# Kernel optimization log

Hardware: AMD Instinct MI355X
Metric: run time of the kernel (lower is better)

## Reference

```python
import jax, jax.numpy as jnp
import numpy as np

GRID = (8, 8)
EPS = 1e-5  # nn.BatchNorm2d default eps


def _per_tile(t, g, b, w, cb):
    # t: (B, C, th, tw); training-mode BatchNorm over (B, th, tw) per channel
    mean = t.mean(axis=(0, 2, 3))
    var = t.var(axis=(0, 2, 3))  # biased variance, matches torch BN normalization
    xn = (t - mean[:, None, None]) * jax.lax.rsqrt(var[:, None, None] + EPS)
    h = jax.nn.relu(xn * g[:, None, None] + b[:, None, None])
    y = jax.lax.conv_general_dilated(
        h, w, window_strides=(1, 1), padding='SAME',
        dimension_numbers=('NCHW', 'OIHW', 'NCHW'))
    return y + cb[:, None, None] + t  # conv bias + residual


def setup_inputs() -> dict:
    key = jax.random.key(0)
    k1, k2 = jax.random.split(key)
    B, C, H, W = 32, 32, 160, 160
    n_tiles = GRID[0] * GRID[1]
    x = jax.random.normal(k1, (B, C, H, W), dtype=jnp.float32)
    gamma = jnp.ones((n_tiles, C), dtype=jnp.float32)
    beta = jnp.zeros((n_tiles, C), dtype=jnp.float32)
    # kaiming-ish init for 3x3 conv
    conv_w = jax.random.normal(k2, (n_tiles, C, C, 3, 3), dtype=jnp.float32) * (2.0 / (C * 9)) ** 0.5
    conv_b = jnp.zeros((n_tiles, C), dtype=jnp.float32)
    return {"x": x, "gamma": gamma, "beta": beta, "conv_w": conv_w, "conv_b": conv_b}


def reference(x, gamma, beta, conv_w, conv_b):
    B, C, H, W = x.shape
    gi, gj = GRID
    th, tw = H // gi, W // gj
    # split into (gi*gj, B, C, th, tw) tiles
    tiles = x.reshape(B, C, gi, th, gj, tw).transpose(2, 4, 0, 1, 3, 5)
    tiles = tiles.reshape(gi * gj, B, C, th, tw)
    out = jax.vmap(_per_tile)(tiles, gamma, beta, conv_w, conv_b)
    # reassemble
    out = out.reshape(gi, gj, B, C, th, tw).transpose(2, 3, 0, 4, 1, 5)
    return out.reshape(B, C, H, W)
```

## Files before the change

kernel.cpp:

```cpp
#include <hip/hip_runtime.h>

#define NT 64
#define B_ 32
#define C_ 32
#define H_ 160
#define W_ 160
#define TH 20
#define TW 20
#define NPIX (TH*TW)
#define NRED (B_*NPIX)
#define EPS 1e-5f

typedef __bf16 bf16x8 __attribute__((ext_vector_type(8)));
typedef float  f32x4  __attribute__((ext_vector_type(4)));

__global__ __launch_bounds__(320) void statsA_kernel(const float* __restrict__ x,
                                                     float* __restrict__ ppS,
                                                     float* __restrict__ ppS2) {
    int blk = blockIdx.x;
    int b = blk >> 5;
    int c = blk & 31;
    const float* plane = x + ((long)(b*C_ + c)) * H_ * W_;

    int tid = threadIdx.x;
    int col4 = tid % 40;
    int tc   = col4 / 5;
    int rbase = tid / 40;

    __shared__ float sh[320], sh2[320], shr[64], shr2[64];

    for (int tr = 0; tr < 8; ++tr) {
        float s = 0.f, s2 = 0.f;
        #pragma unroll
        for (int k = 0; k < 3; ++k) {
            int i = tid + 320*k;
            if (i < 800) {
                int row = tr*20 + rbase + 8*k;
                const float* p = plane + row*W_ + col4*4;
                float4 v = *(const float4*)p;
                s  += v.x + v.y + v.z + v.w;
                s2 += v.x*v.x + v.y*v.y + v.z*v.z + v.w*v.w;
            }
        }
        sh[tid] = s; sh2[tid] = s2;
        __syncthreads();
        if (tid < 64) {
            int tcc = tid >> 3, sl = tid & 7;
            float ps = 0.f, ps2 = 0.f;
            #pragma unroll
            for (int r = 0; r < 5; ++r) {
                int t = sl*40 + tcc*5 + r;
                ps += sh[t]; ps2 += sh2[t];
            }
            shr[tid] = ps; shr2[tid] = ps2;
        }
        __syncthreads();
        if (tid < 8) {
            float ps = 0.f, ps2 = 0.f;
            #pragma unroll
            for (int sl = 0; sl < 8; ++sl) { ps += shr[tid*8 + sl]; ps2 += shr2[tid*8 + sl]; }
            int tl = tr*8 + tid;
            atomicAdd(&ppS [tl*C_ + c], ps);
            atomicAdd(&ppS2[tl*C_ + c], ps2);
        }
        __syncthreads();
    }
}

__global__ __launch_bounds__(512, 4) void fused_kernel(
        const float* __restrict__ x,
        const float* __restrict__ gamma,
        const float* __restrict__ beta,
        const float* __restrict__ conv_w,
        const float* __restrict__ conv_b,
        const float* __restrict__ ppS,
        const float* __restrict__ ppS2,
        float* __restrict__ out) {
    int blk = blockIdx.x;
    int tl = blk >> 5;
    int b  = blk & 31;
    int ti = (tl >> 3) * TH;
    int tj = (tl & 7)  * TW;
    int tid = threadIdx.x;

    __shared__ __align__(16) unsigned char smem[75776];
    __bf16* hlds  = (__bf16*)smem;
    __bf16* wlds  = (__bf16*)(smem + 30976);
    __bf16* obuf  = (__bf16*)(smem + 49408);
    float*  scale = (float*)(smem + 75520);
    float*  shiftv= (float*)(smem + 75648);

    {
        unsigned int* hz = (unsigned int*)smem;
        for (int i = tid; i < 7744; i += 512) hz[i] = 0u;
    }
    if (tid < C_) {
        int c = tid;
        float s  = ppS [tl*C_ + c];
        float s2 = ppS2[tl*C_ + c];
        float m  = s / (float)NRED;
        float var = s2 / (float)NRED - m*m;
        float rs = rsqrtf(var + EPS);
        float g  = gamma[tl*C_ + c];
        scale[c]  = g * rs;
        shiftv[c] = beta[tl*C_ + c] - m * rs * g;
    }
    {
        const float* wsrc = conv_w + (long)tl * C_ * C_ * 9;
        for (int f = tid; f < C_*C_*9; f += 512) {
            int co  = f / 288;
            int rem = f - co*288;
            int cin = rem / 9;
            int tap = rem - cin*9;
            wlds[(tap*C_ + co)*C_ + cin] = (__bf16)wsrc[f];
        }
    }
    __syncthreads();

    for (int idx = tid; idx < C_*TH*5; idx += 512) {
        int c   = idx / 100;
        int rem = idx - c*100;
        int y   = rem / 5;
        int x4  = rem - y*5;
        const float* p = x + ((long)(b*C_ + c)*H_ + ti + y)*W_ + tj + x4*4;
        float4 v = *(const float4*)p;
        float sc = scale[c], sf = shiftv[c];
        int base = ((y+1)*22 + (x4*4 + 1)) * C_ + c;
        hlds[base        ] = (__bf16)fmaxf(v.x*sc + sf, 0.f);
        hlds[base + C_   ] = (__bf16)fmaxf(v.y*sc + sf, 0.f);
        hlds[base + 2*C_ ] = (__bf16)fmaxf(v.z*sc + sf, 0.f);
        hlds[base + 3*C_ ] = (__bf16)fmaxf(v.w*sc + sf, 0.f);
    }
    __syncthreads();

    int wv   = tid >> 6;
    int lane = tid & 63;
    int mm   = lane & 15;
    int j0   = (lane >> 4) * 8;

    bf16x8 bfr[9][2];
    #pragma unroll
    for (int tap = 0; tap < 9; ++tap) {
        #pragma unroll
        for (int h = 0; h < 2; ++h)
            bfr[tap][h] = *(const bf16x8*)&wlds[(tap*C_ + (h*16 + mm))*C_ + j0];
    }
    float b0 = conv_b[tl*C_ + mm];
    float b1 = conv_b[tl*C_ + 16 + mm];

    for (int chunk = wv; chunk < 25; chunk += 8) {
        int p  = chunk*16 + mm;
        int py = p / 20;
        int px = p - py*20;
        f32x4 a0, a1;
        #pragma unroll
        for (int r = 0; r < 4; ++r) { a0[r] = b0; a1[r] = b1; }
        #pragma unroll
        for (int ky = 0; ky < 3; ++ky) {
            #pragma unroll
            for (int kx = 0; kx < 3; ++kx) {
                bf16x8 af = *(const bf16x8*)&hlds[((py+ky)*22 + (px+kx))*C_ + j0];
                a0 = __builtin_amdgcn_mfma_f32_16x16x32_bf16(af, bfr[ky*3+kx][0], a0, 0, 0, 0);
                a1 = __builtin_amdgcn_mfma_f32_16x16x32_bf16(af, bfr[ky*3+kx][1], a1, 0, 0, 0);
            }
        }
        #pragma unroll
        for (int r = 0; r < 4; ++r) {
            int pix = chunk*16 + (lane >> 4)*4 + r;
            obuf[mm*408 + pix]        = (__bf16)a0[r];
            obuf[(16 + mm)*408 + pix] = (__bf16)a1[r];
        }
    }
    __syncthreads();

    for (int idx = tid; idx < C_*NPIX; idx += 512) {
        int co = idx / NPIX;
        int p  = idx - co*NPIX;
        int y  = p / 20;
        int xx = p - y*20;
        long o = ((long)(b*C_ + co)*H_ + ti + y)*W_ + tj + xx;
        out[o] = (float)obuf[co*408 + p] + x[o];
    }
}

extern "C" void kernel_launch(void* const* d_in, const int* in_sizes, int n_in,
                              void* d_out, int out_size, void* d_ws, size_t ws_size,
                              hipStream_t stream) {
    const float* x      = (const float*)d_in[0];
    const float* gamma  = (const float*)d_in[1];
    const float* beta   = (const float*)d_in[2];
    const float* conv_w = (const float*)d_in[3];
    const float* conv_b = (const float*)d_in[4];
    float* out = (float*)d_out;

    float* ppS  = (float*)d_ws;
    float* ppS2 = ppS + NT*C_;

    hipMemsetAsync(d_ws, 0, 2 * NT * C_ * sizeof(float), stream);
    statsA_kernel<<<B_ * C_, 320, 0, stream>>>(x, ppS, ppS2);
    fused_kernel<<<NT * B_, 512, 0, stream>>>(x, gamma, beta, conv_w, conv_b,
                                              ppS, ppS2, out);
}
```

Baseline: 301.3 us.

## Pad LDS strides, alias weight/output buffers, vectorize epilogue and stats reduction

```diff
diff --git a/kernel.cpp b/kernel.cpp
--- a/kernel.cpp
+++ b/kernel.cpp
@@ -11,7 +11,11 @@
 #define NRED (B_*NPIX)
 #define EPS 1e-5f
 
+#define HP 40
+#define OP 404
+
 typedef __bf16 bf16x8 __attribute__((ext_vector_type(8)));
+typedef __bf16 bf16x4 __attribute__((ext_vector_type(4)));
 typedef float  f32x4  __attribute__((ext_vector_type(4)));
 
 __global__ __launch_bounds__(320) void statsA_kernel(const float* __restrict__ x,
@@ -22,48 +26,44 @@
     int c = blk & 31;
     const float* plane = x + ((long)(b*C_ + c)) * H_ * W_;
 
-    int tid = threadIdx.x;
-    int col4 = tid % 40;
-    int tc   = col4 / 5;
+    int tid   = threadIdx.x;
+    int col4  = tid % 40;
     int rbase = tid / 40;
 
-    __shared__ float sh[320], sh2[320], shr[64], shr2[64];
-
+    __shared__ float sh [8 * 321];
+    __shared__ float sh2[8 * 321];
+
+    #pragma unroll
     for (int tr = 0; tr < 8; ++tr) {
         float s = 0.f, s2 = 0.f;
         #pragma unroll
         for (int k = 0; k < 3; ++k) {
-            int i = tid + 320*k;
-            if (i < 800) {
-                int row = tr*20 + rbase + 8*k;
-                const float* p = plane + row*W_ + col4*4;
-                float4 v = *(const float4*)p;
+            int r20 = rbase + 8*k;
+            if (r20 < 20) {
+                int row = tr*20 + r20;
+                float4 v = *(const float4*)(plane + row*W_ + col4*4);
                 s  += v.x + v.y + v.z + v.w;
                 s2 += v.x*v.x + v.y*v.y + v.z*v.z + v.w*v.w;
             }
         }
-        sh[tid] = s; sh2[tid] = s2;
-        __syncthreads();
-        if (tid < 64) {
-            int tcc = tid >> 3, sl = tid & 7;
-            float ps = 0.f, ps2 = 0.f;
+        sh [tr*321 + tid] = s;
+        sh2[tr*321 + tid] = s2;
+    }
+    __syncthreads();
+
+    if (tid < 64) {
+        int tr = tid >> 3, tc = tid & 7;
+        float ps = 0.f, ps2 = 0.f;
+        #pragma unroll
+        for (int rb = 0; rb < 8; ++rb)
             #pragma unroll
-            for (int r = 0; r < 5; ++r) {
-                int t = sl*40 + tcc*5 + r;
+            for (int c5 = 0; c5 < 5; ++c5) {
+                int t = tr*321 + rb*40 + tc*5 + c5;
                 ps += sh[t]; ps2 += sh2[t];
             }
-            shr[tid] = ps; shr2[tid] = ps2;
-        }
-        __syncthreads();
-        if (tid < 8) {
-            float ps = 0.f, ps2 = 0.f;
-            #pragma unroll
-            for (int sl = 0; sl < 8; ++sl) { ps += shr[tid*8 + sl]; ps2 += shr2[tid*8 + sl]; }
-            int tl = tr*8 + tid;
-            atomicAdd(&ppS [tl*C_ + c], ps);
-            atomicAdd(&ppS2[tl*C_ + c], ps2);
-        }
-        __syncthreads();
+        int tl = tr*8 + tc;
+        atomicAdd(&ppS [tl*C_ + c], ps);
+        atomicAdd(&ppS2[tl*C_ + c], ps2);
     }
 }
 
@@ -83,25 +83,25 @@
     int tj = (tl & 7)  * TW;
     int tid = threadIdx.x;
 
-    __shared__ __align__(16) unsigned char smem[75776];
-    __bf16* hlds  = (__bf16*)smem;
-    __bf16* wlds  = (__bf16*)(smem + 30976);
-    __bf16* obuf  = (__bf16*)(smem + 49408);
-    float*  scale = (float*)(smem + 75520);
-    float*  shiftv= (float*)(smem + 75648);
+    __shared__ __align__(16) unsigned char smem[64832];
+    __bf16* hlds   = (__bf16*)smem;
+    __bf16* wlds   = (__bf16*)(smem + 38720);
+    __bf16* obuf   = (__bf16*)(smem + 38720);
+    float*  scale  = (float*)(smem + 64576);
+    float*  shiftv = (float*)(smem + 64704);
 
     {
-        unsigned int* hz = (unsigned int*)smem;
-        for (int i = tid; i < 7744; i += 512) hz[i] = 0u;
+        uint4* hz = (uint4*)smem;
+        for (int i = tid; i < 2420; i += 512) hz[i] = uint4{0,0,0,0};
     }
     if (tid < C_) {
         int c = tid;
-        float s  = ppS [tl*C_ + c];
-        float s2 = ppS2[tl*C_ + c];
-        float m  = s / (float)NRED;
+        float s   = ppS [tl*C_ + c];
+        float s2  = ppS2[tl*C_ + c];
+        float m   = s / (float)NRED;
         float var = s2 / (float)NRED - m*m;
-        float rs = rsqrtf(var + EPS);
-        float g  = gamma[tl*C_ + c];
+        float rs  = rsqrtf(var + EPS);
+        float g   = gamma[tl*C_ + c];
         scale[c]  = g * rs;
         shiftv[c] = beta[tl*C_ + c] - m * rs * g;
     }
@@ -112,7 +112,7 @@
             int rem = f - co*288;
             int cin = rem / 9;
             int tap = rem - cin*9;
-            wlds[(tap*C_ + co)*C_ + cin] = (__bf16)wsrc[f];
+            wlds[(tap*C_ + co)*HP + cin] = (__bf16)wsrc[f];
         }
     }
     __syncthreads();
@@ -125,28 +125,30 @@
         const float* p = x + ((long)(b*C_ + c)*H_ + ti + y)*W_ + tj + x4*4;
         float4 v = *(const float4*)p;
         float sc = scale[c], sf = shiftv[c];
-        int base = ((y+1)*22 + (x4*4 + 1)) * C_ + c;
-        hlds[base        ] = (__bf16)fmaxf(v.x*sc + sf, 0.f);
-        hlds[base + C_   ] = (__bf16)fmaxf(v.y*sc + sf, 0.f);
-        hlds[base + 2*C_ ] = (__bf16)fmaxf(v.z*sc + sf, 0.f);
-        hlds[base + 3*C_ ] = (__bf16)fmaxf(v.w*sc + sf, 0.f);
-    }
-    __syncthreads();
-
+        int base = ((y+1)*22 + (x4*4 + 1)) * HP + c;
+        hlds[base         ] = (__bf16)fmaxf(v.x*sc + sf, 0.f);
+        hlds[base +   HP  ] = (__bf16)fmaxf(v.y*sc + sf, 0.f);
+        hlds[base + 2*HP  ] = (__bf16)fmaxf(v.z*sc + sf, 0.f);
+        hlds[base + 3*HP  ] = (__bf16)fmaxf(v.w*sc + sf, 0.f);
+    }
+    __syncthreads();
+
+    int lane = tid & 63;
     int wv   = tid >> 6;
-    int lane = tid & 63;
     int mm   = lane & 15;
-    int j0   = (lane >> 4) * 8;
+    int jg   = lane >> 4;
+    int j0   = jg * 8;
 
     bf16x8 bfr[9][2];
     #pragma unroll
     for (int tap = 0; tap < 9; ++tap) {
         #pragma unroll
         for (int h = 0; h < 2; ++h)
-            bfr[tap][h] = *(const bf16x8*)&wlds[(tap*C_ + (h*16 + mm))*C_ + j0];
+            bfr[tap][h] = *(const bf16x8*)&wlds[(tap*C_ + (h*16 + mm))*HP + j0];
     }
     float b0 = conv_b[tl*C_ + mm];
     float b1 = conv_b[tl*C_ + 16 + mm];
+    __syncthreads();
 
     for (int chunk = wv; chunk < 25; chunk += 8) {
         int p  = chunk*16 + mm;
@@ -159,27 +161,34 @@
         for (int ky = 0; ky < 3; ++ky) {
             #pragma unroll
             for (int kx = 0; kx < 3; ++kx) {
-                bf16x8 af = *(const bf16x8*)&hlds[((py+ky)*22 + (px+kx))*C_ + j0];
+                bf16x8 af = *(const bf16x8*)&hlds[((py+ky)*22 + (px+kx))*HP + j0];
                 a0 = __builtin_amdgcn_mfma_f32_16x16x32_bf16(af, bfr[ky*3+kx][0], a0, 0, 0, 0);
                 a1 = __builtin_amdgcn_mfma_f32_16x16x32_bf16(af, bfr[ky*3+kx][1], a1, 0, 0, 0);
             }
         }
-        #pragma unroll
-        for (int r = 0; r < 4; ++r) {
-            int pix = chunk*16 + (lane >> 4)*4 + r;
-            obuf[mm*408 + pix]        = (__bf16)a0[r];
-            obuf[(16 + mm)*408 + pix] = (__bf16)a1[r];
-        }
-    }
-    __syncthreads();
-
-    for (int idx = tid; idx < C_*NPIX; idx += 512) {
-        int co = idx / NPIX;
-        int p  = idx - co*NPIX;
-        int y  = p / 20;
-        int xx = p - y*20;
-        long o = ((long)(b*C_ + co)*H_ + ti + y)*W_ + tj + xx;
-        out[o] = (float)obuf[co*408 + p] + x[o];
+        bf16x4 o0, o1;
+        #pragma unroll
+        for (int r = 0; r < 4; ++r) { o0[r] = (__bf16)a0[r]; o1[r] = (__bf16)a1[r]; }
+        int pb = chunk*16 + jg*4;
+        *(bf16x4*)&obuf[mm*OP + pb]        = o0;
+        *(bf16x4*)&obuf[(16 + mm)*OP + pb] = o1;
+    }
+    __syncthreads();
+
+    for (int idx = tid; idx < C_*NPIX/4; idx += 512) {
+        int co = idx / 100;
+        int q  = idx - co*100;
+        int y  = q / 5;
+        int x4 = q - y*5;
+        bf16x4 v = *(const bf16x4*)&obuf[co*OP + y*20 + x4*4];
+        long o = (((long)(b*C_ + co))*H_ + ti + y)*W_ + tj + x4*4;
+        float4 xr = *(const float4*)&x[o];
+        float4 ov;
+        ov.x = (float)v[0] + xr.x;
+        ov.y = (float)v[1] + xr.y;
+        ov.z = (float)v[2] + xr.z;
+        ov.w = (float)v[3] + xr.w;
+        *(float4*)&out[o] = ov;
     }
 }
 
```

Measured after the change: 273.8 us. 9.1% less time.
